# Performance work log

Measured on AMD Instinct MI355X. Metric: run time of the kernel, lower is better.

Reference implementation:

```python
import jax, jax.numpy as jnp
import numpy as np

RADIUS = 0.1
NSAMPLE = 32


def ball_query_cnt(radius, nsample, xyz, new_xyz):
    """xyz: (B,N,3), new_xyz: (B,npoint,3) -> cnt (B,npoint) int32, idx (B,npoint,nsample) int32.
    Matches pointnet2 CUDA semantics: first `nsample` in-radius points in index order;
    unfilled slots replicate the first found index (0 if none found)."""
    N = xyz.shape[1]
    # (B, npoint, N) squared distances
    d2 = jnp.sum((new_xyz[:, :, None, :] - xyz[:, None, :, :]) ** 2, axis=-1)
    mask = d2 < radius * radius
    pos = jnp.arange(N, dtype=jnp.int32)
    # key encodes position so that top_k returns the LOWEST valid positions first
    key = jnp.where(mask, N - pos, -N)
    topk_vals, _ = jax.lax.top_k(key, nsample)          # (B, npoint, nsample)
    valid = topk_vals > 0
    idx = (N - topk_vals).astype(jnp.int32)
    first = jnp.where(valid[..., :1], idx[..., :1], 0)   # fill value per query
    idx = jnp.where(valid, idx, first)
    cnt = jnp.minimum(mask.sum(axis=-1), nsample).astype(jnp.int32)
    return cnt, idx


def group(features, idx):
    """features: (B,C,N), idx: (B,npoint,nsample) -> (B,C,npoint,nsample)."""
    return jax.vmap(lambda f, i: f[:, i])(features, idx)


def setup_inputs() -> dict:
    key = jax.random.key(0)
    k1, k2, k3 = jax.random.split(key, 3)
    B, N, npoint, C = 4, 16384, 2048, 64
    xyz = jax.random.uniform(k1, (B, N, 3), dtype=jnp.float32)
    new_xyz = jax.random.uniform(k2, (B, npoint, 3), dtype=jnp.float32)
    features = jax.random.normal(k3, (B, C, N), dtype=jnp.float32)
    return {"xyz": xyz, "new_xyz": new_xyz, "features": features}


def reference(xyz, new_xyz, features):
    idx_cnt, idx = ball_query_cnt(RADIUS, NSAMPLE, xyz, new_xyz)
    xyz_t = jnp.transpose(xyz, (0, 2, 1))                      # (B,3,N)
    grouped_xyz = group(xyz_t, idx)                            # (B,3,npoint,nsample)
    grouped_xyz = grouped_xyz - jnp.transpose(new_xyz, (0, 2, 1))[..., None]
    grouped_features = group(features, idx)                    # (B,C,npoint,nsample)
    new_features = jnp.concatenate([grouped_xyz, grouped_features], axis=1)
    return idx_cnt, new_features
```

## Files before the change

kernel.cpp:

```cpp
#include <hip/hip_runtime.h>

#define B        4
#define N        16384
#define NPOINT   2048
#define C        64
#define NSAMPLE  32
#define CH       (C + 3)
#define RADIUS2  0.01f
#define NCELL    1000
#define CSTRIDE  1032
#define CCSTRIDE 1024
#define CAP      256

__device__ __forceinline__ int clamp10(int v) {
    return v < 0 ? 0 : (v > 9 ? 9 : v);
}

__global__ __launch_bounds__(256) void zero_kernel(int* __restrict__ p, int n) {
    const int i = blockIdx.x * 256 + threadIdx.x;
    if (i < n) p[i] = 0;
}

__global__ __launch_bounds__(256) void count_kernel(const float* __restrict__ xyz,
                                                    int* __restrict__ cnt) {
    const int g = blockIdx.x * 256 + threadIdx.x;
    const int b = g >> 14;
    const float x = xyz[g * 3 + 0], y = xyz[g * 3 + 1], z = xyz[g * 3 + 2];
    const int cx = clamp10((int)(x * 10.f));
    const int cy = clamp10((int)(y * 10.f));
    const int cz = clamp10((int)(z * 10.f));
    atomicAdd(&cnt[(b << 10) + (cx * 10 + cy) * 10 + cz], 1);
}

__global__ __launch_bounds__(1024) void prefix_kernel(int* __restrict__ cnt,
                                                      int* __restrict__ cs) {
    __shared__ int s[1024];
    const int t = threadIdx.x, b = blockIdx.x;
    const int v = (t < NCELL) ? cnt[(b << 10) + t] : 0;
    s[t] = v;
    __syncthreads();
    for (int off = 1; off < 1024; off <<= 1) {
        const int u = (t >= off) ? s[t - off] : 0;
        __syncthreads();
        s[t] += u;
        __syncthreads();
    }
    const int excl = (t == 0) ? 0 : s[t - 1];
    if (t <= NCELL) cs[b * CSTRIDE + t] = excl;
    if (t < NCELL)  cnt[(b << 10) + t] = excl;
}

__global__ __launch_bounds__(256) void scatter_kernel(const float* __restrict__ xyz,
                                                      int* __restrict__ cursor,
                                                      float4* __restrict__ sp) {
    const int g = blockIdx.x * 256 + threadIdx.x;
    const int b = g >> 14;
    const int n = g & (N - 1);
    const float x = xyz[g * 3 + 0], y = xyz[g * 3 + 1], z = xyz[g * 3 + 2];
    const int cx = clamp10((int)(x * 10.f));
    const int cy = clamp10((int)(y * 10.f));
    const int cz = clamp10((int)(z * 10.f));
    const int cell = (cx * 10 + cy) * 10 + cz;
    const int pos = atomicAdd(&cursor[(b << 10) + cell], 1);
    sp[(b << 14) + pos] = make_float4(x, y, z, __int_as_float(n));
}

__global__ __launch_bounds__(256) void feat_transpose_kernel(
    const float* __restrict__ f,
    float* __restrict__ ft)
{
    __shared__ float tile[64][65];
    const int b  = blockIdx.y;
    const int n0 = blockIdx.x * 64;
    const int t  = threadIdx.x;
    const int r16 = t >> 4;
    const int x4  = t & 15;
    #pragma unroll
    for (int it = 0; it < 4; ++it) {
        const int cc = it * 16 + r16;
        const float4 v = *(const float4*)(f + ((size_t)b * C + cc) * N + n0 + x4 * 4);
        tile[cc][x4 * 4 + 0] = v.x;
        tile[cc][x4 * 4 + 1] = v.y;
        tile[cc][x4 * 4 + 2] = v.z;
        tile[cc][x4 * 4 + 3] = v.w;
    }
    __syncthreads();
    #pragma unroll
    for (int it = 0; it < 4; ++it) {
        const int nn = it * 16 + r16;
        float4 v;
        v.x = tile[x4 * 4 + 0][nn];
        v.y = tile[x4 * 4 + 1][nn];
        v.z = tile[x4 * 4 + 2][nn];
        v.w = tile[x4 * 4 + 3][nn];
        *(float4*)(ft + ((size_t)b * N + n0 + nn) * C + x4 * 4) = v;
    }
}

__global__ __launch_bounds__(64) void qg_grid_kernel(
    const float*  __restrict__ xyz,
    const float*  __restrict__ new_xyz,
    const float*  __restrict__ ft,
    const int*    __restrict__ cs,
    const float4* __restrict__ sp,
    float* __restrict__ out_cnt,
    float* __restrict__ out_feat)
{
    const int q = blockIdx.x;
    const int b = q >> 11;
    const int j = q & (NPOINT - 1);
    const int l = threadIdx.x;

    __shared__ int   cand[CAP];
    __shared__ int   s_idx[NSAMPLE];
    __shared__ float s_tile[CH * 33];

    const float qx = new_xyz[q * 3 + 0];
    const float qy = new_xyz[q * 3 + 1];
    const float qz = new_xyz[q * 3 + 2];

    const int cx = clamp10((int)(qx * 10.f));
    const int cy = clamp10((int)(qy * 10.f));
    const int cz = clamp10((int)(qz * 10.f));
    const int z0 = cz > 0 ? cz - 1 : 0;
    const int z1 = cz < 9 ? cz + 1 : 9;

    int sv = 0, ev = 0;
    if (l < 9) {
        const int xx = cx - 1 + l / 3;
        const int yy = cy - 1 + l % 3;
        if (xx >= 0 && xx <= 9 && yy >= 0 && yy <= 9) {
            const int cb = (xx * 10 + yy) * 10;
            sv = cs[b * CSTRIDE + cb + z0];
            ev = cs[b * CSTRIDE + cb + z1 + 1];
        }
    }

    const unsigned long long ltmask = (1ull << l) - 1ull;
    int total = 0, ncand = 0;
    for (int r = 0; r < 9; ++r) {
        const int rs = __shfl(sv, r);
        const int re = __shfl(ev, r);
        for (int p0 = rs; p0 < re; p0 += 64) {
            const int p = p0 + l;
            const bool act = p < re;
            float4 pt = make_float4(1e9f, 1e9f, 1e9f, 0.f);
            if (act) pt = sp[(b << 14) + p];
            const float dx = pt.x - qx, dy = pt.y - qy, dz = pt.z - qz;
            const float d2 = dx * dx + dy * dy + dz * dz;
            const bool in = act && (d2 < RADIUS2);
            const unsigned long long m = __ballot(in);
            if (in) {
                const int slot = ncand + __popcll(m & ltmask);
                if (slot < CAP) cand[slot] = __float_as_int(pt.w);
            }
            const int c = __popcll(m);
            total += c;
            ncand = ncand + c > CAP ? CAP : ncand + c;
        }
    }

    int cntv;
    if (total > CAP) {
        const float* xb = xyz + (size_t)b * N * 3;
        int cnt2 = 0;
        for (int base = 0; base < N; base += 64) {
            const int p = base + l;
            const float dx = xb[p * 3 + 0] - qx;
            const float dy = xb[p * 3 + 1] - qy;
            const float dz = xb[p * 3 + 2] - qz;
            const float d2 = dx * dx + dy * dy + dz * dz;
            const bool in = d2 < RADIUS2;
            const unsigned long long m = __ballot(in);
            if (in) {
                const int slot = cnt2 + __popcll(m & ltmask);
                if (slot < NSAMPLE) s_idx[slot] = p;
            }
            cnt2 += __popcll(m);
            if (cnt2 >= NSAMPLE) break;
        }
        cntv = cnt2 < NSAMPLE ? cnt2 : NSAMPLE;
        __syncthreads();
    } else {
        __syncthreads();
        const int K = ncand;
        for (int c = l; c < K; c += 64) {
            const int v = cand[c];
            int rnk = 0;
            for (int i = 0; i < K; ++i) rnk += (cand[i] < v) ? 1 : 0;
            if (rnk < NSAMPLE) s_idx[rnk] = v;
        }
        cntv = total < NSAMPLE ? total : NSAMPLE;
        __syncthreads();
    }

    if (l == 0) out_cnt[q] = (float)cntv;
    if (l < NSAMPLE && l >= cntv) s_idx[l] = (cntv > 0) ? s_idx[0] : 0;
    __syncthreads();

    #pragma unroll
    for (int p = 0; p < 8; ++p) {
        const int k  = p * 4 + (l >> 4);
        const int c4 = l & 15;
        const int i  = s_idx[k];
        const float4 v = ((const float4*)(ft + ((size_t)b * N + i) * C))[c4];
        const int ch = 3 + c4 * 4;
        s_tile[(ch + 0) * 33 + k] = v.x;
        s_tile[(ch + 1) * 33 + k] = v.y;
        s_tile[(ch + 2) * 33 + k] = v.z;
        s_tile[(ch + 3) * 33 + k] = v.w;
    }
    if (l < NSAMPLE) {
        const int i = s_idx[l];
        const float* xp = xyz + ((size_t)b * N + i) * 3;
        s_tile[0 * 33 + l] = xp[0] - qx;
        s_tile[1 * 33 + l] = xp[1] - qy;
        s_tile[2 * 33 + l] = xp[2] - qz;
    }
    __syncthreads();

    float4* of4 = (float4*)out_feat;
    for (int e4 = l; e4 < CH * 8; e4 += 64) {
        const int ch = e4 >> 3;
        const int k4 = e4 & 7;
        float4 v;
        v.x = s_tile[ch * 33 + k4 * 4 + 0];
        v.y = s_tile[ch * 33 + k4 * 4 + 1];
        v.z = s_tile[ch * 33 + k4 * 4 + 2];
        v.w = s_tile[ch * 33 + k4 * 4 + 3];
        of4[((size_t)(b * CH + ch) * NPOINT + j) * 8 + k4] = v;
    }
}

template <bool TRANSPOSED>
__global__ __launch_bounds__(64) void qg_wave_kernel(
    const float* __restrict__ xyz,
    const float* __restrict__ new_xyz,
    const float* __restrict__ feat,
    float* __restrict__ out_cnt,
    float* __restrict__ out_feat)
{
    const int q = blockIdx.x;
    const int b = q >> 11;
    const int j = q & (NPOINT - 1);
    const int l = threadIdx.x;

    __shared__ int   s_idx[NSAMPLE];
    __shared__ float s_tile[CH * 33];

    const float qx = new_xyz[q * 3 + 0];
    const float qy = new_xyz[q * 3 + 1];
    const float qz = new_xyz[q * 3 + 2];
    const float* xb = xyz + (size_t)b * N * 3;

    int cnt = 0;
    for (int base = 0; base < N; base += 64) {
        const int p = base + l;
        const float dx = xb[p * 3 + 0] - qx;
        const float dy = xb[p * 3 + 1] - qy;
        const float dz = xb[p * 3 + 2] - qz;
        const float d2 = dx * dx + dy * dy + dz * dz;
        const bool in = d2 < RADIUS2;
        const unsigned long long m = __ballot(in);
        if (in) {
            const int slot = cnt + __popcll(m & ((1ull << l) - 1ull));
            if (slot < NSAMPLE) s_idx[slot] = p;
        }
        cnt += __popcll(m);
        if (cnt >= NSAMPLE) break;
    }
    if (cnt > NSAMPLE) cnt = NSAMPLE;

    if (l == 0) out_cnt[q] = (float)cnt;
    __syncthreads();
    if (l < NSAMPLE && l >= cnt) s_idx[l] = (cnt > 0) ? s_idx[0] : 0;
    __syncthreads();

    #pragma unroll
    for (int p = 0; p < 8; ++p) {
        const int k  = p * 4 + (l >> 4);
        const int c4 = l & 15;
        const int i  = s_idx[k];
        if (TRANSPOSED) {
            const float4 v = ((const float4*)(feat + ((size_t)b * N + i) * C))[c4];
            const int ch = 3 + c4 * 4;
            s_tile[(ch + 0) * 33 + k] = v.x;
            s_tile[(ch + 1) * 33 + k] = v.y;
            s_tile[(ch + 2) * 33 + k] = v.z;
            s_tile[(ch + 3) * 33 + k] = v.w;
        } else {
            #pragma unroll
            for (int cc = 0; cc < 4; ++cc) {
                const int c = c4 * 4 + cc;
                s_tile[(3 + c) * 33 + k] = feat[((size_t)b * C + c) * N + i];
            }
        }
    }
    if (l < NSAMPLE) {
        const int i = s_idx[l];
        const float* xp = xyz + ((size_t)b * N + i) * 3;
        s_tile[0 * 33 + l] = xp[0] - qx;
        s_tile[1 * 33 + l] = xp[1] - qy;
        s_tile[2 * 33 + l] = xp[2] - qz;
    }
    __syncthreads();

    float4* of4 = (float4*)out_feat;
    for (int e4 = l; e4 < CH * 8; e4 += 64) {
        const int ch = e4 >> 3;
        const int k4 = e4 & 7;
        float4 v;
        v.x = s_tile[ch * 33 + k4 * 4 + 0];
        v.y = s_tile[ch * 33 + k4 * 4 + 1];
        v.z = s_tile[ch * 33 + k4 * 4 + 2];
        v.w = s_tile[ch * 33 + k4 * 4 + 3];
        of4[((size_t)(b * CH + ch) * NPOINT + j) * 8 + k4] = v;
    }
}

extern "C" void kernel_launch(void* const* d_in, const int* in_sizes, int n_in,
                              void* d_out, int out_size, void* d_ws, size_t ws_size,
                              hipStream_t stream) {
    const float* xyz      = (const float*)d_in[0];
    const float* new_xyz  = (const float*)d_in[1];
    const float* features = (const float*)d_in[2];

    float* out_cnt  = (float*)d_out;
    float* out_feat = out_cnt + (size_t)B * NPOINT;

    char* ws = (char*)d_ws;
    const size_t ftB = (size_t)B * N * C * sizeof(float);
    const size_t spB = (size_t)B * N * sizeof(float4);
    const size_t csB = (size_t)B * CSTRIDE * sizeof(int);
    const size_t ccB = (size_t)B * CCSTRIDE * sizeof(int);
    const size_t need = ftB + spB + csB + ccB;

    if (ws_size >= need) {
        float*  ft = (float*)ws;
        float4* sp = (float4*)(ws + ftB);
        int*    cs = (int*)(ws + ftB + spB);
        int*    cc = (int*)(ws + ftB + spB + csB);
        zero_kernel<<<(B * CCSTRIDE + 255) / 256, 256, 0, stream>>>(cc, B * CCSTRIDE);
        count_kernel<<<B * N / 256, 256, 0, stream>>>(xyz, cc);
        prefix_kernel<<<B, 1024, 0, stream>>>(cc, cs);
        scatter_kernel<<<B * N / 256, 256, 0, stream>>>(xyz, cc, sp);
        feat_transpose_kernel<<<dim3(N / 64, B), 256, 0, stream>>>(features, ft);
        qg_grid_kernel<<<B * NPOINT, 64, 0, stream>>>(xyz, new_xyz, ft, cs, sp,
                                                      out_cnt, out_feat);
    } else if (ws_size >= ftB) {
        float* ft = (float*)ws;
        feat_transpose_kernel<<<dim3(N / 64, B), 256, 0, stream>>>(features, ft);
        qg_wave_kernel<true><<<B * NPOINT, 64, 0, stream>>>(xyz, new_xyz, ft,
                                                            out_cnt, out_feat);
    } else {
        qg_wave_kernel<false><<<B * NPOINT, 64, 0, stream>>>(xyz, new_xyz, features,
                                                             out_cnt, out_feat);
    }
}
```

Measured before the change: 126.0 us.

## Split query kernel into select and gather, fuse count with transpose, shuffle prefix

Merges the cell-count and feature-transpose kernels into one prep launch and rewrites the prefix scan to use wave shuffles instead of a log-step shared-memory scan with many barriers. The per-query grid kernel is split into a select kernel, which writes neighbour indices to a workspace buffer, and a separate gather kernel. Both pack four queries per 256-thread block to raise occupancy. This costs an extra launch, an index round trip through global memory, and a larger workspace requirement. The old path is kept as a fallback when the workspace is too small.

```diff
diff --git a/kernel.cpp b/kernel.cpp
--- a/kernel.cpp
+++ b/kernel.cpp
@@ -12,6 +12,8 @@
 #define CCSTRIDE 1024
 #define CAP      256
 
+#define WAVE_FENCE() asm volatile("s_waitcnt lgkmcnt(0)" ::: "memory")
+
 __device__ __forceinline__ int clamp10(int v) {
     return v < 0 ? 0 : (v > 9 ? 9 : v);
 }
@@ -21,9 +23,8 @@
     if (i < n) p[i] = 0;
 }
 
-__global__ __launch_bounds__(256) void count_kernel(const float* __restrict__ xyz,
-                                                    int* __restrict__ cnt) {
-    const int g = blockIdx.x * 256 + threadIdx.x;
+__device__ __forceinline__ void count_body(const float* __restrict__ xyz,
+                                           int* __restrict__ cnt, int g) {
     const int b = g >> 14;
     const float x = xyz[g * 3 + 0], y = xyz[g * 3 + 1], z = xyz[g * 3 + 2];
     const int cx = clamp10((int)(x * 10.f));
@@ -32,20 +33,79 @@
     atomicAdd(&cnt[(b << 10) + (cx * 10 + cy) * 10 + cz], 1);
 }
 
+__device__ __forceinline__ void transpose_body(const float* __restrict__ f,
+                                               float* __restrict__ ft,
+                                               int n0, int b, int t,
+                                               float (*tile)[65]) {
+    const int r16 = t >> 4;
+    const int x4  = t & 15;
+    #pragma unroll
+    for (int it = 0; it < 4; ++it) {
+        const int cc = it * 16 + r16;
+        const float4 v = *(const float4*)(f + ((size_t)b * C + cc) * N + n0 + x4 * 4);
+        tile[cc][x4 * 4 + 0] = v.x;
+        tile[cc][x4 * 4 + 1] = v.y;
+        tile[cc][x4 * 4 + 2] = v.z;
+        tile[cc][x4 * 4 + 3] = v.w;
+    }
+    __syncthreads();
+    #pragma unroll
+    for (int it = 0; it < 4; ++it) {
+        const int nn = it * 16 + r16;
+        float4 v;
+        v.x = tile[x4 * 4 + 0][nn];
+        v.y = tile[x4 * 4 + 1][nn];
+        v.z = tile[x4 * 4 + 2][nn];
+        v.w = tile[x4 * 4 + 3][nn];
+        *(float4*)(ft + ((size_t)b * N + n0 + nn) * C + x4 * 4) = v;
+    }
+}
+
+__global__ __launch_bounds__(256) void prep_kernel(const float* __restrict__ xyz,
+                                                   int* __restrict__ cnt,
+                                                   const float* __restrict__ f,
+                                                   float* __restrict__ ft) {
+    __shared__ float tile[64][65];
+    if (blockIdx.x < (B * N / 256)) {
+        count_body(xyz, cnt, blockIdx.x * 256 + threadIdx.x);
+    } else {
+        const int bi = blockIdx.x - (B * N / 256);
+        transpose_body(f, ft, (bi & 255) * 64, bi >> 8, threadIdx.x, tile);
+    }
+}
+
+__global__ __launch_bounds__(256) void feat_transpose_kernel(
+    const float* __restrict__ f, float* __restrict__ ft) {
+    __shared__ float tile[64][65];
+    transpose_body(f, ft, blockIdx.x * 64, blockIdx.y, threadIdx.x, tile);
+}
+
 __global__ __launch_bounds__(1024) void prefix_kernel(int* __restrict__ cnt,
                                                       int* __restrict__ cs) {
-    __shared__ int s[1024];
+    __shared__ int wsum[16];
     const int t = threadIdx.x, b = blockIdx.x;
+    const int w = t >> 6, l = t & 63;
     const int v = (t < NCELL) ? cnt[(b << 10) + t] : 0;
-    s[t] = v;
-    __syncthreads();
-    for (int off = 1; off < 1024; off <<= 1) {
-        const int u = (t >= off) ? s[t - off] : 0;
-        __syncthreads();
-        s[t] += u;
-        __syncthreads();
-    }
-    const int excl = (t == 0) ? 0 : s[t - 1];
+    int inc = v;
+    #pragma unroll
+    for (int off = 1; off < 64; off <<= 1) {
+        const int u = __shfl_up(inc, off);
+        if (l >= off) inc += u;
+    }
+    if (l == 63) wsum[w] = inc;
+    __syncthreads();
+    if (t < 16) {
+        int s = wsum[t];
+        #pragma unroll
+        for (int off = 1; off < 16; off <<= 1) {
+            const int u = __shfl_up(s, off, 16);
+            if (t >= off) s += u;
+        }
+        wsum[t] = s;
+    }
+    __syncthreads();
+    const int base = (w > 0) ? wsum[w - 1] : 0;
+    const int excl = base + inc - v;
     if (t <= NCELL) cs[b * CSTRIDE + t] = excl;
     if (t < NCELL)  cnt[(b << 10) + t] = excl;
 }
@@ -65,55 +125,21 @@
     sp[(b << 14) + pos] = make_float4(x, y, z, __int_as_float(n));
 }
 
-__global__ __launch_bounds__(256) void feat_transpose_kernel(
-    const float* __restrict__ f,
-    float* __restrict__ ft)
-{
-    __shared__ float tile[64][65];
-    const int b  = blockIdx.y;
-    const int n0 = blockIdx.x * 64;
-    const int t  = threadIdx.x;
-    const int r16 = t >> 4;
-    const int x4  = t & 15;
-    #pragma unroll
-    for (int it = 0; it < 4; ++it) {
-        const int cc = it * 16 + r16;
-        const float4 v = *(const float4*)(f + ((size_t)b * C + cc) * N + n0 + x4 * 4);
-        tile[cc][x4 * 4 + 0] = v.x;
-        tile[cc][x4 * 4 + 1] = v.y;
-        tile[cc][x4 * 4 + 2] = v.z;
-        tile[cc][x4 * 4 + 3] = v.w;
-    }
-    __syncthreads();
-    #pragma unroll
-    for (int it = 0; it < 4; ++it) {
-        const int nn = it * 16 + r16;
-        float4 v;
-        v.x = tile[x4 * 4 + 0][nn];
-        v.y = tile[x4 * 4 + 1][nn];
-        v.z = tile[x4 * 4 + 2][nn];
-        v.w = tile[x4 * 4 + 3][nn];
-        *(float4*)(ft + ((size_t)b * N + n0 + nn) * C + x4 * 4) = v;
-    }
-}
-
-__global__ __launch_bounds__(64) void qg_grid_kernel(
+__global__ __launch_bounds__(256, 8) void select_kernel(
     const float*  __restrict__ xyz,
     const float*  __restrict__ new_xyz,
-    const float*  __restrict__ ft,
     const int*    __restrict__ cs,
     const float4* __restrict__ sp,
     float* __restrict__ out_cnt,
-    float* __restrict__ out_feat)
+    int*   __restrict__ idxg)
 {
-    const int q = blockIdx.x;
+    const int w = threadIdx.x >> 6;
+    const int l = threadIdx.x & 63;
+    const int q = blockIdx.x * 4 + w;
     const int b = q >> 11;
-    const int j = q & (NPOINT - 1);
-    const int l = threadIdx.x;
-
-    __shared__ int   cand[CAP];
-    __shared__ int   s_idx[NSAMPLE];
-    __shared__ float s_tile[CH * 33];
+
+    __shared__ int cand_s[4][CAP];
+    int* cand = cand_s[w];
 
     const float qx = new_xyz[q * 3 + 0];
     const float qy = new_xyz[q * 3 + 1];
@@ -159,6 +185,199 @@
             ncand = ncand + c > CAP ? CAP : ncand + c;
         }
     }
+    WAVE_FENCE();
+
+    int cntv;
+    if (total > CAP) {
+        const float* xb = xyz + (size_t)b * N * 3;
+        int cnt2 = 0;
+        for (int base = 0; base < N; base += 64) {
+            const int p = base + l;
+            const float dx = xb[p * 3 + 0] - qx;
+            const float dy = xb[p * 3 + 1] - qy;
+            const float dz = xb[p * 3 + 2] - qz;
+            const float d2 = dx * dx + dy * dy + dz * dz;
+            const bool in = d2 < RADIUS2;
+            const unsigned long long m = __ballot(in);
+            if (in) {
+                const int slot = cnt2 + __popcll(m & ltmask);
+                if (slot < NSAMPLE) idxg[q * NSAMPLE + slot] = p;
+            }
+            cnt2 += __popcll(m);
+            if (cnt2 >= NSAMPLE) break;
+        }
+        cntv = cnt2 < NSAMPLE ? cnt2 : NSAMPLE;
+    } else {
+        const int K = ncand;
+        for (int c = l; c < K; c += 64) {
+            const int v = cand[c];
+            int rnk = 0;
+            for (int i = 0; i < K; ++i) rnk += (cand[i] < v) ? 1 : 0;
+            if (rnk < NSAMPLE) idxg[q * NSAMPLE + rnk] = v;
+        }
+        cntv = total < NSAMPLE ? total : NSAMPLE;
+    }
+    if (l == 0) out_cnt[q] = (float)cntv;
+}
+
+__global__ __launch_bounds__(256, 8) void gather_kernel(
+    const float* __restrict__ xyz,
+    const float* __restrict__ new_xyz,
+    const float* __restrict__ ft,
+    const float* __restrict__ out_cnt,
+    const int*   __restrict__ idxg,
+    float* __restrict__ out_feat)
+{
+    const int w = threadIdx.x >> 6;
+    const int l = threadIdx.x & 63;
+    const int q = blockIdx.x * 4 + w;
+    const int b = q >> 11;
+    const int j = q & (NPOINT - 1);
+
+    __shared__ int   s_i_s[4][NSAMPLE];
+    __shared__ float tile_s[4][35 * 33];
+    int*   s_i  = s_i_s[w];
+    float* tile = tile_s[w];
+
+    const int cnt = (int)out_cnt[q];
+    const float qx = new_xyz[q * 3 + 0];
+    const float qy = new_xyz[q * 3 + 1];
+    const float qz = new_xyz[q * 3 + 2];
+
+    if (l < NSAMPLE) {
+        int fv = 0;
+        if (cnt > 0) fv = idxg[q * NSAMPLE];
+        s_i[l] = (l < cnt) ? idxg[q * NSAMPLE + l] : fv;
+    }
+    __syncthreads();
+
+    if (l < NSAMPLE) {
+        const int i = s_i[l];
+        const float* xp = xyz + ((size_t)b * N + i) * 3;
+        tile[0 * 33 + l] = xp[0] - qx;
+        tile[1 * 33 + l] = xp[1] - qy;
+        tile[2 * 33 + l] = xp[2] - qz;
+    }
+    const float4* ft4 = (const float4*)ft;
+    #pragma unroll
+    for (int t = 0; t < 4; ++t) {
+        const int k  = t * 8 + (l >> 3);
+        const int c4 = l & 7;
+        const float4 v = ft4[((size_t)b * N + s_i[k]) * (C / 4) + c4];
+        const int ch = 3 + c4 * 4;
+        tile[(ch + 0) * 33 + k] = v.x;
+        tile[(ch + 1) * 33 + k] = v.y;
+        tile[(ch + 2) * 33 + k] = v.z;
+        tile[(ch + 3) * 33 + k] = v.w;
+    }
+    __syncthreads();
+
+    float4* of4 = (float4*)out_feat;
+    #pragma unroll
+    for (int t = 0; t < 5; ++t) {
+        const int e4 = t * 64 + l;
+        if (e4 < 35 * 8) {
+            const int ch = e4 >> 3;
+            const int k4 = e4 & 7;
+            float4 v;
+            v.x = tile[ch * 33 + k4 * 4 + 0];
+            v.y = tile[ch * 33 + k4 * 4 + 1];
+            v.z = tile[ch * 33 + k4 * 4 + 2];
+            v.w = tile[ch * 33 + k4 * 4 + 3];
+            of4[((size_t)(b * CH + ch) * NPOINT + j) * 8 + k4] = v;
+        }
+    }
+    __syncthreads();
+
+    #pragma unroll
+    for (int t = 0; t < 4; ++t) {
+        const int k  = t * 8 + (l >> 3);
+        const int c4 = 8 + (l & 7);
+        const float4 v = ft4[((size_t)b * N + s_i[k]) * (C / 4) + c4];
+        const int r = (c4 - 8) * 4;
+        tile[(r + 0) * 33 + k] = v.x;
+        tile[(r + 1) * 33 + k] = v.y;
+        tile[(r + 2) * 33 + k] = v.z;
+        tile[(r + 3) * 33 + k] = v.w;
+    }
+    __syncthreads();
+
+    #pragma unroll
+    for (int t = 0; t < 4; ++t) {
+        const int e4  = t * 64 + l;
+        const int chr = e4 >> 3;
+        const int k4  = e4 & 7;
+        float4 v;
+        v.x = tile[chr * 33 + k4 * 4 + 0];
+        v.y = tile[chr * 33 + k4 * 4 + 1];
+        v.z = tile[chr * 33 + k4 * 4 + 2];
+        v.w = tile[chr * 33 + k4 * 4 + 3];
+        of4[((size_t)(b * CH + 35 + chr) * NPOINT + j) * 8 + k4] = v;
+    }
+}
+
+__global__ __launch_bounds__(64) void qg_grid_kernel(
+    const float*  __restrict__ xyz,
+    const float*  __restrict__ new_xyz,
+    const float*  __restrict__ ft,
+    const int*    __restrict__ cs,
+    const float4* __restrict__ sp,
+    float* __restrict__ out_cnt,
+    float* __restrict__ out_feat)
+{
+    const int q = blockIdx.x;
+    const int b = q >> 11;
+    const int j = q & (NPOINT - 1);
+    const int l = threadIdx.x;
+
+    __shared__ int   cand[CAP];
+    __shared__ int   s_idx[NSAMPLE];
+    __shared__ float s_tile[CH * 33];
+
+    const float qx = new_xyz[q * 3 + 0];
+    const float qy = new_xyz[q * 3 + 1];
+    const float qz = new_xyz[q * 3 + 2];
+
+    const int cx = clamp10((int)(qx * 10.f));
+    const int cy = clamp10((int)(qy * 10.f));
+    const int cz = clamp10((int)(qz * 10.f));
+    const int z0 = cz > 0 ? cz - 1 : 0;
+    const int z1 = cz < 9 ? cz + 1 : 9;
+
+    int sv = 0, ev = 0;
+    if (l < 9) {
+        const int xx = cx - 1 + l / 3;
+        const int yy = cy - 1 + l % 3;
+        if (xx >= 0 && xx <= 9 && yy >= 0 && yy <= 9) {
+            const int cb = (xx * 10 + yy) * 10;
+            sv = cs[b * CSTRIDE + cb + z0];
+            ev = cs[b * CSTRIDE + cb + z1 + 1];
+        }
+    }
+
+    const unsigned long long ltmask = (1ull << l) - 1ull;
+    int total = 0, ncand = 0;
+    for (int r = 0; r < 9; ++r) {
+        const int rs = __shfl(sv, r);
+        const int re = __shfl(ev, r);
+        for (int p0 = rs; p0 < re; p0 += 64) {
+            const int p = p0 + l;
+            const bool act = p < re;
+            float4 pt = make_float4(1e9f, 1e9f, 1e9f, 0.f);
+            if (act) pt = sp[(b << 14) + p];
+            const float dx = pt.x - qx, dy = pt.y - qy, dz = pt.z - qz;
+            const float d2 = dx * dx + dy * dy + dz * dz;
+            const bool in = act && (d2 < RADIUS2);
+            const unsigned long long m = __ballot(in);
+            if (in) {
+                const int slot = ncand + __popcll(m & ltmask);
+                if (slot < CAP) cand[slot] = __float_as_int(pt.w);
+            }
+            const int c = __popcll(m);
+            total += c;
+            ncand = ncand + c > CAP ? CAP : ncand + c;
+        }
+    }
 
     int cntv;
     if (total > CAP) {
@@ -329,24 +548,35 @@
     float* out_feat = out_cnt + (size_t)B * NPOINT;
 
     char* ws = (char*)d_ws;
-    const size_t ftB = (size_t)B * N * C * sizeof(float);
-    const size_t spB = (size_t)B * N * sizeof(float4);
-    const size_t csB = (size_t)B * CSTRIDE * sizeof(int);
-    const size_t ccB = (size_t)B * CCSTRIDE * sizeof(int);
-    const size_t need = ftB + spB + csB + ccB;
-
-    if (ws_size >= need) {
-        float*  ft = (float*)ws;
-        float4* sp = (float4*)(ws + ftB);
-        int*    cs = (int*)(ws + ftB + spB);
-        int*    cc = (int*)(ws + ftB + spB + csB);
+    const size_t ftB  = (size_t)B * N * C * sizeof(float);
+    const size_t spB  = (size_t)B * N * sizeof(float4);
+    const size_t csB  = (size_t)B * CSTRIDE * sizeof(int);
+    const size_t ccB  = (size_t)B * CCSTRIDE * sizeof(int);
+    const size_t idxB = (size_t)B * NPOINT * NSAMPLE * sizeof(int);
+    const size_t need_old = ftB + spB + csB + ccB;
+    const size_t need_new = need_old + idxB;
+
+    if (ws_size >= need_old) {
+        float*  ft  = (float*)ws;
+        float4* sp  = (float4*)(ws + ftB);
+        int*    cs  = (int*)(ws + ftB + spB);
+        int*    cc  = (int*)(ws + ftB + spB + csB);
+        int*    idxg = (int*)(ws + ftB + spB + csB + ccB);
+
         zero_kernel<<<(B * CCSTRIDE + 255) / 256, 256, 0, stream>>>(cc, B * CCSTRIDE);
-        count_kernel<<<B * N / 256, 256, 0, stream>>>(xyz, cc);
+        prep_kernel<<<(B * N / 256) + (N / 64) * B, 256, 0, stream>>>(xyz, cc,
+                                                                      features, ft);
         prefix_kernel<<<B, 1024, 0, stream>>>(cc, cs);
         scatter_kernel<<<B * N / 256, 256, 0, stream>>>(xyz, cc, sp);
-        feat_transpose_kernel<<<dim3(N / 64, B), 256, 0, stream>>>(features, ft);
-        qg_grid_kernel<<<B * NPOINT, 64, 0, stream>>>(xyz, new_xyz, ft, cs, sp,
-                                                      out_cnt, out_feat);
+        if (ws_size >= need_new) {
+            select_kernel<<<B * NPOINT / 4, 256, 0, stream>>>(xyz, new_xyz, cs, sp,
+                                                              out_cnt, idxg);
+            gather_kernel<<<B * NPOINT / 4, 256, 0, stream>>>(xyz, new_xyz, ft,
+                                                              out_cnt, idxg, out_feat);
+        } else {
+            qg_grid_kernel<<<B * NPOINT, 64, 0, stream>>>(xyz, new_xyz, ft, cs, sp,
+                                                          out_cnt, out_feat);
+        }
     } else if (ws_size >= ftB) {
         float* ft = (float*)ws;
         feat_transpose_kernel<<<dim3(N / 64, B), 256, 0, stream>>>(features, ft);
```

After: 128.9 us. 2.3% more time.

## Fuse grid-build and transpose into one prep kernel, pack four queries per block

Applied to the files above, without the earlier changes.

Replaces the zero, count, prefix and scatter kernels with one shared-memory grid builder per batch that runs in the same launch as the feature transpose. The query kernel now packs four independent wavefront queries into a 256-thread block and uses wave-level LDS fences instead of block barriers. Its output tile is split into two halves to shrink LDS per wave. This removes several launches and global atomics at the cost of a serialized per-batch grid build on only four blocks, and it depends on wavefront-synchronous assumptions.

```diff
diff --git a/kernel.cpp b/kernel.cpp
--- a/kernel.cpp
+++ b/kernel.cpp
@@ -9,70 +9,23 @@
 #define RADIUS2  0.01f
 #define NCELL    1000
 #define CSTRIDE  1032
-#define CCSTRIDE 1024
 #define CAP      256
+
+#define WAVE_FENCE() asm volatile("s_waitcnt lgkmcnt(0)" ::: "memory")
 
 __device__ __forceinline__ int clamp10(int v) {
     return v < 0 ? 0 : (v > 9 ? 9 : v);
 }
 
-__global__ __launch_bounds__(256) void zero_kernel(int* __restrict__ p, int n) {
-    const int i = blockIdx.x * 256 + threadIdx.x;
-    if (i < n) p[i] = 0;
-}
-
-__global__ __launch_bounds__(256) void count_kernel(const float* __restrict__ xyz,
-                                                    int* __restrict__ cnt) {
-    const int g = blockIdx.x * 256 + threadIdx.x;
-    const int b = g >> 14;
-    const float x = xyz[g * 3 + 0], y = xyz[g * 3 + 1], z = xyz[g * 3 + 2];
-    const int cx = clamp10((int)(x * 10.f));
-    const int cy = clamp10((int)(y * 10.f));
-    const int cz = clamp10((int)(z * 10.f));
-    atomicAdd(&cnt[(b << 10) + (cx * 10 + cy) * 10 + cz], 1);
-}
-
-__global__ __launch_bounds__(1024) void prefix_kernel(int* __restrict__ cnt,
-                                                      int* __restrict__ cs) {
-    __shared__ int s[1024];
-    const int t = threadIdx.x, b = blockIdx.x;
-    const int v = (t < NCELL) ? cnt[(b << 10) + t] : 0;
-    s[t] = v;
-    __syncthreads();
-    for (int off = 1; off < 1024; off <<= 1) {
-        const int u = (t >= off) ? s[t - off] : 0;
-        __syncthreads();
-        s[t] += u;
-        __syncthreads();
-    }
-    const int excl = (t == 0) ? 0 : s[t - 1];
-    if (t <= NCELL) cs[b * CSTRIDE + t] = excl;
-    if (t < NCELL)  cnt[(b << 10) + t] = excl;
-}
-
-__global__ __launch_bounds__(256) void scatter_kernel(const float* __restrict__ xyz,
-                                                      int* __restrict__ cursor,
-                                                      float4* __restrict__ sp) {
-    const int g = blockIdx.x * 256 + threadIdx.x;
-    const int b = g >> 14;
-    const int n = g & (N - 1);
-    const float x = xyz[g * 3 + 0], y = xyz[g * 3 + 1], z = xyz[g * 3 + 2];
-    const int cx = clamp10((int)(x * 10.f));
-    const int cy = clamp10((int)(y * 10.f));
-    const int cz = clamp10((int)(z * 10.f));
-    const int cell = (cx * 10 + cy) * 10 + cz;
-    const int pos = atomicAdd(&cursor[(b << 10) + cell], 1);
-    sp[(b << 14) + pos] = make_float4(x, y, z, __int_as_float(n));
-}
-
-__global__ __launch_bounds__(256) void feat_transpose_kernel(
-    const float* __restrict__ f,
-    float* __restrict__ ft)
-{
-    __shared__ float tile[64][65];
-    const int b  = blockIdx.y;
-    const int n0 = blockIdx.x * 64;
-    const int t  = threadIdx.x;
+__device__ __forceinline__ int cell_of(float x, float y, float z) {
+    return (clamp10((int)(x * 10.f)) * 10 + clamp10((int)(y * 10.f))) * 10
+         + clamp10((int)(z * 10.f));
+}
+
+__device__ __forceinline__ void transpose_body(const float* __restrict__ f,
+                                               float* __restrict__ ft,
+                                               int n0, int b, int t,
+                                               float (*tile)[65]) {
     const int r16 = t >> 4;
     const int x4  = t & 15;
     #pragma unroll
@@ -97,7 +50,79 @@
     }
 }
 
-__global__ __launch_bounds__(64) void qg_grid_kernel(
+__global__ __launch_bounds__(256) void prep2_kernel(
+    const float*  __restrict__ xyz,
+    const float*  __restrict__ f,
+    float*        __restrict__ ft,
+    int*          __restrict__ cs,
+    float4*       __restrict__ sp)
+{
+    __shared__ int   cnts[1024];
+    __shared__ int   wsum[4];
+    __shared__ float tile[64][65];
+    const int t = threadIdx.x;
+
+    if (blockIdx.x < B) {
+        const int b = blockIdx.x;
+        const float* xb = xyz + (size_t)b * N * 3;
+
+        for (int i = t; i < 1024; i += 256) cnts[i] = 0;
+        __syncthreads();
+
+        for (int i = t; i < N; i += 256) {
+            const float x = xb[i * 3 + 0], y = xb[i * 3 + 1], z = xb[i * 3 + 2];
+            atomicAdd(&cnts[cell_of(x, y, z)], 1);
+        }
+        __syncthreads();
+
+        const int base4 = t * 4;
+        const int a0 = cnts[base4 + 0], a1 = cnts[base4 + 1];
+        const int a2 = cnts[base4 + 2], a3 = cnts[base4 + 3];
+        const int s  = a0 + a1 + a2 + a3;
+        const int w  = t >> 6, l = t & 63;
+        int inc = s;
+        #pragma unroll
+        for (int off = 1; off < 64; off <<= 1) {
+            const int u = __shfl_up(inc, off);
+            if (l >= off) inc += u;
+        }
+        if (l == 63) wsum[w] = inc;
+        __syncthreads();
+        int wbase = 0;
+        #pragma unroll
+        for (int k = 0; k < 4; ++k) wbase += (k < w) ? wsum[k] : 0;
+        const int e0 = wbase + inc - s;
+        const int e1 = e0 + a0, e2 = e1 + a1, e3 = e2 + a2;
+        cnts[base4 + 0] = e0;
+        cnts[base4 + 1] = e1;
+        cnts[base4 + 2] = e2;
+        cnts[base4 + 3] = e3;
+        int* csb = cs + b * CSTRIDE;
+        csb[base4 + 0] = e0;
+        csb[base4 + 1] = e1;
+        csb[base4 + 2] = e2;
+        csb[base4 + 3] = e3;
+        __syncthreads();
+
+        float4* spb = sp + ((size_t)b << 14);
+        for (int i = t; i < N; i += 256) {
+            const float x = xb[i * 3 + 0], y = xb[i * 3 + 1], z = xb[i * 3 + 2];
+            const int pos = atomicAdd(&cnts[cell_of(x, y, z)], 1);
+            spb[pos] = make_float4(x, y, z, __int_as_float(i));
+        }
+    } else {
+        const int bi = blockIdx.x - B;
+        transpose_body(f, ft, (bi & 255) * 64, bi >> 8, t, tile);
+    }
+}
+
+__global__ __launch_bounds__(256) void feat_transpose_kernel(
+    const float* __restrict__ f, float* __restrict__ ft) {
+    __shared__ float tile[64][65];
+    transpose_body(f, ft, blockIdx.x * 64, blockIdx.y, threadIdx.x, tile);
+}
+
+__global__ __launch_bounds__(256, 6) void qg_fused_kernel(
     const float*  __restrict__ xyz,
     const float*  __restrict__ new_xyz,
     const float*  __restrict__ ft,
@@ -106,14 +131,18 @@
     float* __restrict__ out_cnt,
     float* __restrict__ out_feat)
 {
-    const int q = blockIdx.x;
+    const int w = threadIdx.x >> 6;
+    const int l = threadIdx.x & 63;
+    const int q = blockIdx.x * 4 + w;
     const int b = q >> 11;
     const int j = q & (NPOINT - 1);
-    const int l = threadIdx.x;
-
-    __shared__ int   cand[CAP];
-    __shared__ int   s_idx[NSAMPLE];
-    __shared__ float s_tile[CH * 33];
+
+    __shared__ int   cand_s[4][CAP];
+    __shared__ int   si_s[4][NSAMPLE];
+    __shared__ float tile_s[4][35 * 33];
+    int*   cand = cand_s[w];
+    int*   s_i  = si_s[w];
+    float* tile = tile_s[w];
 
     const float qx = new_xyz[q * 3 + 0];
     const float qy = new_xyz[q * 3 + 1];
@@ -159,6 +188,7 @@
             ncand = ncand + c > CAP ? CAP : ncand + c;
         }
     }
+    WAVE_FENCE();
 
     int cntv;
     if (total > CAP) {
@@ -174,61 +204,90 @@
             const unsigned long long m = __ballot(in);
             if (in) {
                 const int slot = cnt2 + __popcll(m & ltmask);
-                if (slot < NSAMPLE) s_idx[slot] = p;
+                if (slot < NSAMPLE) s_i[slot] = p;
             }
             cnt2 += __popcll(m);
             if (cnt2 >= NSAMPLE) break;
         }
         cntv = cnt2 < NSAMPLE ? cnt2 : NSAMPLE;
-        __syncthreads();
     } else {
-        __syncthreads();
         const int K = ncand;
         for (int c = l; c < K; c += 64) {
             const int v = cand[c];
             int rnk = 0;
             for (int i = 0; i < K; ++i) rnk += (cand[i] < v) ? 1 : 0;
-            if (rnk < NSAMPLE) s_idx[rnk] = v;
+            if (rnk < NSAMPLE) s_i[rnk] = v;
         }
         cntv = total < NSAMPLE ? total : NSAMPLE;
-        __syncthreads();
-    }
+    }
+    WAVE_FENCE();
 
     if (l == 0) out_cnt[q] = (float)cntv;
-    if (l < NSAMPLE && l >= cntv) s_idx[l] = (cntv > 0) ? s_idx[0] : 0;
-    __syncthreads();
-
-    #pragma unroll
-    for (int p = 0; p < 8; ++p) {
-        const int k  = p * 4 + (l >> 4);
-        const int c4 = l & 15;
-        const int i  = s_idx[k];
-        const float4 v = ((const float4*)(ft + ((size_t)b * N + i) * C))[c4];
+    if (l < NSAMPLE && l >= cntv) s_i[l] = (cntv > 0) ? s_i[0] : 0;
+    WAVE_FENCE();
+
+    if (l < NSAMPLE) {
+        const int i = s_i[l];
+        const float* xp = xyz + ((size_t)b * N + i) * 3;
+        tile[0 * 33 + l] = xp[0] - qx;
+        tile[1 * 33 + l] = xp[1] - qy;
+        tile[2 * 33 + l] = xp[2] - qz;
+    }
+    const float4* ft4 = (const float4*)ft;
+    #pragma unroll
+    for (int t = 0; t < 4; ++t) {
+        const int k  = t * 8 + (l >> 3);
+        const int c4 = l & 7;
+        const float4 v = ft4[((size_t)b * N + s_i[k]) * (C / 4) + c4];
         const int ch = 3 + c4 * 4;
-        s_tile[(ch + 0) * 33 + k] = v.x;
-        s_tile[(ch + 1) * 33 + k] = v.y;
-        s_tile[(ch + 2) * 33 + k] = v.z;
-        s_tile[(ch + 3) * 33 + k] = v.w;
-    }
-    if (l < NSAMPLE) {
-        const int i = s_idx[l];
-        const float* xp = xyz + ((size_t)b * N + i) * 3;
-        s_tile[0 * 33 + l] = xp[0] - qx;
-        s_tile[1 * 33 + l] = xp[1] - qy;
-        s_tile[2 * 33 + l] = xp[2] - qz;
-    }
-    __syncthreads();
+        tile[(ch + 0) * 33 + k] = v.x;
+        tile[(ch + 1) * 33 + k] = v.y;
+        tile[(ch + 2) * 33 + k] = v.z;
+        tile[(ch + 3) * 33 + k] = v.w;
+    }
+    WAVE_FENCE();
 
     float4* of4 = (float4*)out_feat;
-    for (int e4 = l; e4 < CH * 8; e4 += 64) {
-        const int ch = e4 >> 3;
-        const int k4 = e4 & 7;
+    #pragma unroll
+    for (int t = 0; t < 5; ++t) {
+        const int e4 = t * 64 + l;
+        if (e4 < 35 * 8) {
+            const int ch = e4 >> 3;
+            const int k4 = e4 & 7;
+            float4 v;
+            v.x = tile[ch * 33 + k4 * 4 + 0];
+            v.y = tile[ch * 33 + k4 * 4 + 1];
+            v.z = tile[ch * 33 + k4 * 4 + 2];
+            v.w = tile[ch * 33 + k4 * 4 + 3];
+            of4[((size_t)(b * CH + ch) * NPOINT + j) * 8 + k4] = v;
+        }
+    }
+    WAVE_FENCE();
+
+    #pragma unroll
+    for (int t = 0; t < 4; ++t) {
+        const int k  = t * 8 + (l >> 3);
+        const int c4 = 8 + (l & 7);
+        const float4 v = ft4[((size_t)b * N + s_i[k]) * (C / 4) + c4];
+        const int r = (c4 - 8) * 4;
+        tile[(r + 0) * 33 + k] = v.x;
+        tile[(r + 1) * 33 + k] = v.y;
+        tile[(r + 2) * 33 + k] = v.z;
+        tile[(r + 3) * 33 + k] = v.w;
+    }
+    WAVE_FENCE();
+
+    #pragma unroll
+    for (int t = 0; t < 4; ++t) {
+        const int e4  = t * 64 + l;
+        const int chr = e4 >> 3;
+        const int k4  = e4 & 7;
         float4 v;
-        v.x = s_tile[ch * 33 + k4 * 4 + 0];
-        v.y = s_tile[ch * 33 + k4 * 4 + 1];
-        v.z = s_tile[ch * 33 + k4 * 4 + 2];
-        v.w = s_tile[ch * 33 + k4 * 4 + 3];
-        of4[((size_t)(b * CH + ch) * NPOINT + j) * 8 + k4] = v;
+        v.x = tile[chr * 33 + k4 * 4 + 0];
+        v.y = tile[chr * 33 + k4 * 4 + 1];
+        v.z = tile[chr * 33 + k4 * 4 + 2];
+        v.w = tile[chr * 33 + k4 * 4 + 3];
+        of4[((size_t)(b * CH + 35 + chr) * NPOINT + j) * 8 + k4] = v;
     }
 }
 
@@ -332,21 +391,15 @@
     const size_t ftB = (size_t)B * N * C * sizeof(float);
     const size_t spB = (size_t)B * N * sizeof(float4);
     const size_t csB = (size_t)B * CSTRIDE * sizeof(int);
-    const size_t ccB = (size_t)B * CCSTRIDE * sizeof(int);
-    const size_t need = ftB + spB + csB + ccB;
+    const size_t need = ftB + spB + csB;
 
     if (ws_size >= need) {
         float*  ft = (float*)ws;
         float4* sp = (float4*)(ws + ftB);
         int*    cs = (int*)(ws + ftB + spB);
-        int*    cc = (int*)(ws + ftB + spB + csB);
-        zero_kernel<<<(B * CCSTRIDE + 255) / 256, 256, 0, stream>>>(cc, B * CCSTRIDE);
-        count_kernel<<<B * N / 256, 256, 0, stream>>>(xyz, cc);
-        prefix_kernel<<<B, 1024, 0, stream>>>(cc, cs);
-        scatter_kernel<<<B * N / 256, 256, 0, stream>>>(xyz, cc, sp);
-        feat_transpose_kernel<<<dim3(N / 64, B), 256, 0, stream>>>(features, ft);
-        qg_grid_kernel<<<B * NPOINT, 64, 0, stream>>>(xyz, new_xyz, ft, cs, sp,
-                                                      out_cnt, out_feat);
+        prep2_kernel<<<B + B * (N / 64), 256, 0, stream>>>(xyz, features, ft, cs, sp);
+        qg_fused_kernel<<<B * NPOINT / 4, 256, 0, stream>>>(xyz, new_xyz, ft, cs, sp,
+                                                            out_cnt, out_feat);
     } else if (ws_size >= ftB) {
         float* ft = (float*)ws;
         feat_transpose_kernel<<<dim3(N / 64, B), 256, 0, stream>>>(features, ft);
```

After: 153.8 us. 22.1% more time.
